# Performance work log

Measured on AMD Instinct MI355X. Metric: run time of the kernel, lower is better.

Reference implementation:

```python
import jax, jax.numpy as jnp
import numpy as np

PATCH_RATIO = 0.1
EPS = 1e-8

def _unfold(x, ps):
    # torch F.unfold(kernel=stride=ps): [b,c,H,W] -> [b, c*ps*ps, L], (c,kh,kw)-major channel layout
    b, c, H, W = x.shape
    nh, nw = (H - ps) // ps + 1, (W - ps) // ps + 1
    xc = x[:, :, :nh * ps, :nw * ps].reshape(b, c, nh, ps, nw, ps)
    u = xc.transpose(0, 1, 3, 5, 2, 4).reshape(b, c * ps * ps, nh * nw)
    return u, nh, nw

def _fold(cols, ps, H, W, nh, nw, c):
    # torch F.fold(kernel=stride=ps, output=(H,W)); non-overlapping so no accumulation,
    # uncovered bottom/right border is zero
    b = cols.shape[0]
    y = cols.reshape(b, c, ps, ps, nh, nw).transpose(0, 1, 4, 2, 5, 3)
    y = y.reshape(b, c, nh * ps, nw * ps)
    return jnp.pad(y, ((0, 0), (0, 0), (0, H - nh * ps), (0, W - nw * ps)))

def _forward(x, H, W):
    b, c = x.shape[0], x.shape[1]
    ps = min(int(H * PATCH_RATIO) + 1, int(W * PATCH_RATIO) + 1)
    u, nh, nw = _unfold(x, ps)                       # [b, c*ps*ps, L]
    p = nh * nw
    # faithful replication of the original (layout-scrambling) reshape
    x_p = u.reshape(b, ps * ps, c, p).transpose(0, 3, 2, 1)   # [b, p, c, ps*ps]
    g = jnp.mean(x, axis=(2, 3))                     # GAP -> [b, c]
    # cosine_similarity(x_g expanded, x_p) over flattened (c*ps*ps):
    # expanded gap row = g repeated ps*ps times -> dot = ps_sumfree einsum, ||g_exp|| = ||g||*ps
    dot = jnp.einsum('bpcd,bc->bp', x_p, g)          # [b, p]
    gnorm = jnp.linalg.norm(g, axis=1) * ps          # [b]
    pnorm = jnp.sqrt(jnp.sum(x_p * x_p, axis=(2, 3)))  # [b, p]
    cos = dot / jnp.maximum(gnorm[:, None] * pnorm, EPS)
    idx = jnp.argmax(cos, axis=1)                    # most similar patch (topk k=1)
    ids = jnp.argmin(cos, axis=1)                    # least similar patch (topk of -cos)
    bidx = jnp.arange(b)
    x_p = x_p.at[bidx, idx].set(x_p[bidx, ids])      # scatter swap
    cols = x_p.reshape(b, p, c * ps * ps).transpose(0, 2, 1)  # [b, c*ps*ps, p]
    mask = _fold(cols, ps, H, W, nh, nw, c)          # [b, c, H, W]
    return mask * x

def setup_inputs() -> dict:
    key = jax.random.key(0)
    x = jax.random.normal(key, (2, 256, 512, 512), dtype=jnp.float32)
    return {"x": x, "H": 512, "W": 512}

def reference(x, H, W):
    return _forward(x, H, W)
```

## Files before the change

kernel.cpp:

```cpp
#include <hip/hip_runtime.h>

#define BB 2
#define CC 256
#define HH 512
#define WW 512
#define PS 52
#define NW 9
#define NP 81
#define COV 468
#define PLANE (HH*WW)
#define CHW (CC*PLANE)
#define SP (PS*PS)

__global__ __launch_bounds__(256) void gap_kernel(const float* __restrict__ x,
                                                  float* __restrict__ gsum) {
    int plane = blockIdx.x;
    const float4* p = (const float4*)(x + (size_t)plane * PLANE);
    float acc = 0.f;
    for (int i = threadIdx.x; i < PLANE / 4; i += 256) {
        float4 v = p[i];
        acc += v.x + v.y + v.z + v.w;
    }
    __shared__ float red[256];
    red[threadIdx.x] = acc;
    __syncthreads();
    for (int s = 128; s > 0; s >>= 1) {
        if (threadIdx.x < s) red[threadIdx.x] += red[threadIdx.x + s];
        __syncthreads();
    }
    if (threadIdx.x == 0) gsum[plane] = red[0];
}

__global__ __launch_bounds__(256) void stats_kernel(const float* __restrict__ x,
                                                    float* __restrict__ T,
                                                    float* __restrict__ pn) {
    int cg = blockIdx.x;
    int l  = blockIdx.y;
    int b  = blockIdx.z;
    int ph = l / NW, pw = l - ph * NW;
    int tid = threadIdx.x;
    int wv = tid >> 6;

    __shared__ float Tpart[4][256];
    #pragma unroll
    for (int w = 0; w < 4; w++) Tpart[w][tid] = 0.f;
    __syncthreads();

    float pacc = 0.f;
    const float* base_b = x + (size_t)b * CHW + (size_t)(ph * PS) * WW + (pw * PS);
    for (int ci = 0; ci < 32; ci++) {
        int ch = cg * 32 + ci;
        const float* base = base_b + (size_t)ch * PLANE;
        float a = 0.f;
        for (unsigned s = tid; s < SP; s += 256) {
            unsigned kh = s / PS;
            unsigned kw = s - kh * PS;
            float v = base[kh * WW + kw];
            a += v;
            pacc += v * v;
        }
        int bin = (144 * ch + tid) & 255;
        Tpart[wv][bin] += a;
    }
    __syncthreads();

    float tsum = Tpart[0][tid] + Tpart[1][tid] + Tpart[2][tid] + Tpart[3][tid];
    T[(((size_t)b * NP + l) * 8 + cg) * 256 + tid] = tsum;

    __shared__ float red[256];
    red[tid] = pacc;
    __syncthreads();
    for (int s2 = 128; s2 > 0; s2 >>= 1) {
        if (tid < s2) red[tid] += red[tid + s2];
        __syncthreads();
    }
    if (tid == 0) pn[((size_t)b * NP + l) * 8 + cg] = red[0];
}

__global__ __launch_bounds__(256) void select_kernel(const float* __restrict__ gsum,
                                                     const float* __restrict__ T,
                                                     const float* __restrict__ pn,
                                                     int* __restrict__ sel) {
    int b = blockIdx.x;
    int t = threadIdx.x;
    float g = gsum[b * 256 + t] * (1.0f / PLANE);

    __shared__ float red[256];
    red[t] = g * g;
    __syncthreads();
    for (int s = 128; s > 0; s >>= 1) {
        if (t < s) red[t] += red[t + s];
        __syncthreads();
    }
    float gnorm = sqrtf(red[0]) * (float)PS;
    __syncthreads();

    float best = -1e30f, worst = 1e30f;
    int bi = 0, wi = 0;
    for (int l = 0; l < NP; l++) {
        const float* Tl = T + ((size_t)b * NP + l) * 8 * 256;
        float d = 0.f;
        #pragma unroll
        for (int cg = 0; cg < 8; cg++) d += Tl[cg * 256 + t];
        d *= g;
        red[t] = d;
        __syncthreads();
        for (int s = 128; s > 0; s >>= 1) {
            if (t < s) red[t] += red[t + s];
            __syncthreads();
        }
        if (t == 0) {
            float pacc = 0.f;
            #pragma unroll
            for (int cg = 0; cg < 8; cg++) pacc += pn[((size_t)b * NP + l) * 8 + cg];
            float pnorm = sqrtf(pacc);
            float cosv = red[0] / fmaxf(gnorm * pnorm, 1e-8f);
            if (cosv > best) { best = cosv; bi = l; }
            if (cosv < worst) { worst = cosv; wi = l; }
        }
        __syncthreads();
    }
    if (t == 0) { sel[b * 2 + 0] = bi; sel[b * 2 + 1] = wi; }
}

__global__ __launch_bounds__(256) void apply_kernel(const float* __restrict__ x,
                                                    float* __restrict__ out,
                                                    const int* __restrict__ sel) {
    int tile = blockIdx.x;
    int tc = tile / 43;
    int ts = tile - tc * 43;
    int l = blockIdx.y;
    int b = blockIdx.z;
    int ph = l / NW, pw = l - ph * NW;
    int idx = sel[b * 2 + 0], ids = sel[b * 2 + 1];
    int sl_patch = (l == idx) ? ids : l;
    int sph = sl_patch / NW, spw = sl_patch - sph * NW;

    const float* xb = x + (size_t)b * CHW;
    const float* src_base = xb + (size_t)(sph * PS) * WW + (spw * PS);

    __shared__ float tilebuf[64][65];
    int cb = tc * 64;
    int sb = ts * 64;
    int t = threadIdx.x;

    {
        int cl = t & 63;
        int sr = t >> 6;
        #pragma unroll
        for (int i = 0; i < 16; i++) {
            int s_l = i * 4 + sr;
            int s_g = sb + s_l;
            float v = 0.f;
            if (s_g < SP) {
                unsigned du = (unsigned)s_g * 256u + (unsigned)(cb + cl);
                unsigned chs = du / SP;
                unsigned rem = du - chs * SP;
                unsigned kh = rem / PS;
                unsigned kw = rem - kh * PS;
                v = src_base[(size_t)chs * PLANE + kh * WW + kw];
            }
            tilebuf[s_l][cl] = v;
        }
    }
    __syncthreads();
    {
        int sl = t & 63;
        int cr = t >> 6;
        int s_g = sb + sl;
        if (s_g < SP) {
            unsigned sh = (unsigned)s_g / PS;
            unsigned sw = (unsigned)s_g - sh * PS;
            size_t pos = (size_t)(ph * PS + sh) * WW + (pw * PS + sw);
            #pragma unroll
            for (int i = 0; i < 16; i++) {
                int c_l = i * 4 + cr;
                size_t off = (size_t)(cb + c_l) * PLANE + pos;
                out[(size_t)b * CHW + off] = tilebuf[sl][c_l] * xb[off];
            }
        }
    }
}

__global__ __launch_bounds__(256) void border_kernel(float* __restrict__ out) {
    int plane = blockIdx.y;
    int t = blockIdx.x * 256 + threadIdx.x;
    if (t >= 10780) return;
    float4* p = (float4*)(out + (size_t)plane * PLANE);
    int idx4;
    if (t < 5632) {
        int row = t / 11;
        int col = t - row * 11;
        idx4 = row * 128 + 117 + col;
    } else {
        int t2 = t - 5632;
        int row = t2 / 117;
        int col = t2 - row * 117;
        idx4 = (COV + row) * 128 + col;
    }
    p[idx4] = make_float4(0.f, 0.f, 0.f, 0.f);
}

extern "C" void kernel_launch(void* const* d_in, const int* in_sizes, int n_in,
                              void* d_out, int out_size, void* d_ws, size_t ws_size,
                              hipStream_t stream) {
    const float* x = (const float*)d_in[0];
    float* out = (float*)d_out;
    float* ws = (float*)d_ws;

    float* T    = ws;
    float* pn   = ws + 331776;
    float* gsum = ws + 333072;
    int*   sel  = (int*)(ws + 333584);

    gap_kernel<<<dim3(BB * CC), dim3(256), 0, stream>>>(x, gsum);
    stats_kernel<<<dim3(8, NP, BB), dim3(256), 0, stream>>>(x, T, pn);
    select_kernel<<<dim3(BB), dim3(256), 0, stream>>>(gsum, T, pn, sel);
    apply_kernel<<<dim3(172, NP, BB), dim3(256), 0, stream>>>(x, out, sel);
    border_kernel<<<dim3(43, BB * CC), dim3(256), 0, stream>>>(out);
}
```

Baseline: 1.424 ms.

## Fuse GAP, patch stats, masked output and border zeroing into single pass with fixup

```diff
diff --git a/kernel.cpp b/kernel.cpp
--- a/kernel.cpp
+++ b/kernel.cpp
@@ -12,134 +12,269 @@
 #define CHW (CC*PLANE)
 #define SP (PS*PS)
 
-__global__ __launch_bounds__(256) void gap_kernel(const float* __restrict__ x,
-                                                  float* __restrict__ gsum) {
-    int plane = blockIdx.x;
-    const float4* p = (const float4*)(x + (size_t)plane * PLANE);
-    float acc = 0.f;
-    for (int i = threadIdx.x; i < PLANE / 4; i += 256) {
-        float4 v = p[i];
-        acc += v.x + v.y + v.z + v.w;
-    }
-    __shared__ float red[256];
-    red[threadIdx.x] = acc;
+#define WS_S     0
+#define WS_PN    41472
+#define WS_GSUM  41634
+#define WS_ZTOT  42146
+#define WS_COS   42146
+#define WS_SEL   42308
+
+__global__ __launch_bounds__(256) void zero_kernel(float* __restrict__ ws) {
+    int i = blockIdx.x * 256 + threadIdx.x;
+    if (i < WS_ZTOT) ws[i] = 0.f;
+}
+
+__global__ __launch_bounds__(256) void mega_kernel(const float* __restrict__ x,
+                                                   float* __restrict__ out,
+                                                   float* __restrict__ S,
+                                                   float* __restrict__ pn,
+                                                   float* __restrict__ gsum) {
+    const int cg = blockIdx.x;
+    const int h  = blockIdx.y;
+    const int b  = blockIdx.z;
+    const int t  = threadIdx.x;
+    const int c2 = t >> 4;
+    const int wq = t & 15;
+    const int ch = cg * 16 + c2;
+    const float* xb = x + (size_t)b * CHW;
+    float* ob = out + (size_t)b * CHW;
+
+    const size_t rowoff = (size_t)ch * PLANE + (size_t)h * WW;
+    const float4* xrow = (const float4*)(xb + rowoff);
+    float4* orow = (float4*)(ob + rowoff);
+
+    float gacc = 0.f;
+
+    if (h >= COV) {
+        #pragma unroll
+        for (int i = 0; i < 8; i++) {
+            int w4 = wq + 16 * i;
+            float4 v = xrow[w4];
+            gacc += v.x + v.y + v.z + v.w;
+            orow[w4] = make_float4(0.f, 0.f, 0.f, 0.f);
+        }
+        #pragma unroll
+        for (int o = 8; o > 0; o >>= 1) gacc += __shfl_down(gacc, o, 16);
+        if (wq == 0) atomicAdd(gsum + b * CC + ch, gacc);
+        return;
+    }
+
+    const int ph = h / PS;
+    const int sh = h - ph * PS;
+    const int s0 = sh * PS;
+    const float* prow = xb + (size_t)(ph * PS) * WW;
+
+    float sacc[NW];
+    #pragma unroll
+    for (int p = 0; p < NW; p++) sacc[p] = 0.f;
+    float qacc = 0.f;
+
+    #pragma unroll
+    for (int i = 0; i < 8; i++) {
+        int w4 = wq + 16 * i;
+        float4 v = xrow[w4];
+        gacc += v.x + v.y + v.z + v.w;
+        float4 ov;
+        if (w4 < 117) {
+            float m[4];
+            #pragma unroll
+            for (int j = 0; j < 4; j++) {
+                int w = w4 * 4 + j;
+                int pw = w / PS;
+                int sw = w - pw * PS;
+                unsigned du  = (unsigned)(s0 + sw) * 256u + (unsigned)ch;
+                unsigned chs = du / (unsigned)SP;
+                unsigned rem = du - chs * (unsigned)SP;
+                unsigned kh  = rem / (unsigned)PS;
+                unsigned kw  = rem - kh * (unsigned)PS;
+                float g = prow[(size_t)chs * PLANE + pw * PS + kh * WW + kw];
+                m[j] = g;
+                sacc[pw] += g;
+                qacc += g * g;
+            }
+            ov.x = m[0] * v.x;
+            ov.y = m[1] * v.y;
+            ov.z = m[2] * v.z;
+            ov.w = m[3] * v.w;
+        } else {
+            ov = make_float4(0.f, 0.f, 0.f, 0.f);
+        }
+        orow[w4] = ov;
+    }
+
+    #pragma unroll
+    for (int o = 8; o > 0; o >>= 1) {
+        gacc += __shfl_down(gacc, o, 16);
+        qacc += __shfl_down(qacc, o, 16);
+        #pragma unroll
+        for (int p = 0; p < NW; p++) sacc[p] += __shfl_down(sacc[p], o, 16);
+    }
+    if (wq == 0) {
+        atomicAdd(gsum + b * CC + ch, gacc);
+        #pragma unroll
+        for (int p = 0; p < NW; p++)
+            atomicAdd(S + ((size_t)(b * NP + ph * NW + p)) * 256 + ch, sacc[p]);
+    } else if (wq == 1) {
+    }
+    if (wq == 0) {
+    }
+    (void)0;
+}
+
+
+__global__ __launch_bounds__(256) void mega_kernel2(const float* __restrict__ x,
+                                                    float* __restrict__ out,
+                                                    float* __restrict__ S,
+                                                    float* __restrict__ pn,
+                                                    float* __restrict__ gsum) {
+    const int cg = blockIdx.x;
+    const int h  = blockIdx.y;
+    const int b  = blockIdx.z;
+    const int t  = threadIdx.x;
+    const int c2 = t >> 4;
+    const int wq = t & 15;
+    const int ch = cg * 16 + c2;
+    const float* xb = x + (size_t)b * CHW;
+    float* ob = out + (size_t)b * CHW;
+
+    const size_t rowoff = (size_t)ch * PLANE + (size_t)h * WW;
+    const float4* xrow = (const float4*)(xb + rowoff);
+    float4* orow = (float4*)(ob + rowoff);
+
+    float gacc = 0.f;
+
+    if (h >= COV) {
+        #pragma unroll
+        for (int i = 0; i < 8; i++) {
+            int w4 = wq + 16 * i;
+            float4 v = xrow[w4];
+            gacc += v.x + v.y + v.z + v.w;
+            orow[w4] = make_float4(0.f, 0.f, 0.f, 0.f);
+        }
+        #pragma unroll
+        for (int o = 8; o > 0; o >>= 1) gacc += __shfl_down(gacc, o, 16);
+        if (wq == 0) atomicAdd(gsum + b * CC + ch, gacc);
+        return;
+    }
+
+    const int ph = h / PS;
+    const int sh = h - ph * PS;
+    const int s0 = sh * PS;
+    const float* prow = xb + (size_t)(ph * PS) * WW;
+
+    float sacc[NW], qpat[NW];
+    #pragma unroll
+    for (int p = 0; p < NW; p++) { sacc[p] = 0.f; qpat[p] = 0.f; }
+
+    #pragma unroll
+    for (int i = 0; i < 8; i++) {
+        int w4 = wq + 16 * i;
+        float4 v = xrow[w4];
+        gacc += v.x + v.y + v.z + v.w;
+        float4 ov;
+        if (w4 < 117) {
+            float m[4];
+            #pragma unroll
+            for (int j = 0; j < 4; j++) {
+                int w = w4 * 4 + j;
+                int pw = w / PS;
+                int sw = w - pw * PS;
+                unsigned du  = (unsigned)(s0 + sw) * 256u + (unsigned)ch;
+                unsigned chs = du / (unsigned)SP;
+                unsigned rem = du - chs * (unsigned)SP;
+                unsigned kh  = rem / (unsigned)PS;
+                unsigned kw  = rem - kh * (unsigned)PS;
+                float g = prow[(size_t)chs * PLANE + pw * PS + kh * WW + kw];
+                m[j] = g;
+                sacc[pw] += g;
+                qpat[pw] += g * g;
+            }
+            ov.x = m[0] * v.x;
+            ov.y = m[1] * v.y;
+            ov.z = m[2] * v.z;
+            ov.w = m[3] * v.w;
+        } else {
+            ov = make_float4(0.f, 0.f, 0.f, 0.f);
+        }
+        orow[w4] = ov;
+    }
+
+    #pragma unroll
+    for (int o = 8; o > 0; o >>= 1) {
+        gacc += __shfl_down(gacc, o, 16);
+        #pragma unroll
+        for (int p = 0; p < NW; p++) {
+            sacc[p] += __shfl_down(sacc[p], o, 16);
+            qpat[p] += __shfl_down(qpat[p], o, 16);
+        }
+    }
+    if (wq == 0) {
+        atomicAdd(gsum + b * CC + ch, gacc);
+        size_t Sbase = ((size_t)(b * NP + ph * NW)) * 256 + ch;
+        #pragma unroll
+        for (int p = 0; p < NW; p++) {
+            atomicAdd(S + Sbase + (size_t)p * 256, sacc[p]);
+            atomicAdd(pn + b * NP + ph * NW + p, qpat[p]);
+        }
+    }
+}
+
+__global__ __launch_bounds__(256) void cos_kernel(const float* __restrict__ gsum,
+                                                  const float* __restrict__ S,
+                                                  const float* __restrict__ pn,
+                                                  float* __restrict__ cosv) {
+    int l = blockIdx.x;
+    int b = blockIdx.y;
+    int t = threadIdx.x;
+    float g = gsum[b * CC + t] * (1.0f / PLANE);
+    float d  = S[((size_t)(b * NP + l)) * 256 + t] * g;
+    float gg = g * g;
+    #pragma unroll
+    for (int o = 32; o > 0; o >>= 1) { d += __shfl_down(d, o); gg += __shfl_down(gg, o); }
+    __shared__ float rd[4], rg[4];
+    int wv = t >> 6;
+    if ((t & 63) == 0) { rd[wv] = d; rg[wv] = gg; }
     __syncthreads();
-    for (int s = 128; s > 0; s >>= 1) {
-        if (threadIdx.x < s) red[threadIdx.x] += red[threadIdx.x + s];
-        __syncthreads();
-    }
-    if (threadIdx.x == 0) gsum[plane] = red[0];
-}
-
-__global__ __launch_bounds__(256) void stats_kernel(const float* __restrict__ x,
-                                                    float* __restrict__ T,
-                                                    float* __restrict__ pn) {
-    int cg = blockIdx.x;
-    int l  = blockIdx.y;
-    int b  = blockIdx.z;
-    int ph = l / NW, pw = l - ph * NW;
-    int tid = threadIdx.x;
-    int wv = tid >> 6;
-
-    __shared__ float Tpart[4][256];
-    #pragma unroll
-    for (int w = 0; w < 4; w++) Tpart[w][tid] = 0.f;
-    __syncthreads();
-
-    float pacc = 0.f;
-    const float* base_b = x + (size_t)b * CHW + (size_t)(ph * PS) * WW + (pw * PS);
-    for (int ci = 0; ci < 32; ci++) {
-        int ch = cg * 32 + ci;
-        const float* base = base_b + (size_t)ch * PLANE;
-        float a = 0.f;
-        for (unsigned s = tid; s < SP; s += 256) {
-            unsigned kh = s / PS;
-            unsigned kw = s - kh * PS;
-            float v = base[kh * WW + kw];
-            a += v;
-            pacc += v * v;
-        }
-        int bin = (144 * ch + tid) & 255;
-        Tpart[wv][bin] += a;
-    }
-    __syncthreads();
-
-    float tsum = Tpart[0][tid] + Tpart[1][tid] + Tpart[2][tid] + Tpart[3][tid];
-    T[(((size_t)b * NP + l) * 8 + cg) * 256 + tid] = tsum;
-
-    __shared__ float red[256];
-    red[tid] = pacc;
-    __syncthreads();
-    for (int s2 = 128; s2 > 0; s2 >>= 1) {
-        if (tid < s2) red[tid] += red[tid + s2];
-        __syncthreads();
-    }
-    if (tid == 0) pn[((size_t)b * NP + l) * 8 + cg] = red[0];
-}
-
-__global__ __launch_bounds__(256) void select_kernel(const float* __restrict__ gsum,
-                                                     const float* __restrict__ T,
-                                                     const float* __restrict__ pn,
-                                                     int* __restrict__ sel) {
-    int b = blockIdx.x;
-    int t = threadIdx.x;
-    float g = gsum[b * 256 + t] * (1.0f / PLANE);
-
-    __shared__ float red[256];
-    red[t] = g * g;
-    __syncthreads();
-    for (int s = 128; s > 0; s >>= 1) {
-        if (t < s) red[t] += red[t + s];
-        __syncthreads();
-    }
-    float gnorm = sqrtf(red[0]) * (float)PS;
-    __syncthreads();
-
-    float best = -1e30f, worst = 1e30f;
-    int bi = 0, wi = 0;
-    for (int l = 0; l < NP; l++) {
-        const float* Tl = T + ((size_t)b * NP + l) * 8 * 256;
-        float d = 0.f;
-        #pragma unroll
-        for (int cg = 0; cg < 8; cg++) d += Tl[cg * 256 + t];
-        d *= g;
-        red[t] = d;
-        __syncthreads();
-        for (int s = 128; s > 0; s >>= 1) {
-            if (t < s) red[t] += red[t + s];
-            __syncthreads();
-        }
-        if (t == 0) {
-            float pacc = 0.f;
-            #pragma unroll
-            for (int cg = 0; cg < 8; cg++) pacc += pn[((size_t)b * NP + l) * 8 + cg];
-            float pnorm = sqrtf(pacc);
-            float cosv = red[0] / fmaxf(gnorm * pnorm, 1e-8f);
-            if (cosv > best) { best = cosv; bi = l; }
-            if (cosv < worst) { worst = cosv; wi = l; }
-        }
-        __syncthreads();
-    }
-    if (t == 0) { sel[b * 2 + 0] = bi; sel[b * 2 + 1] = wi; }
-}
-
-__global__ __launch_bounds__(256) void apply_kernel(const float* __restrict__ x,
+    if (t == 0) {
+        float dt = rd[0] + rd[1] + rd[2] + rd[3];
+        float gt = rg[0] + rg[1] + rg[2] + rg[3];
+        float gnorm = sqrtf(gt) * (float)PS;
+        float pnorm = sqrtf(pn[b * NP + l]);
+        cosv[b * NP + l] = dt / fmaxf(gnorm * pnorm, 1e-8f);
+    }
+}
+
+__global__ void sel_kernel(const float* __restrict__ cosv, int* __restrict__ sel) {
+    int b = threadIdx.x;
+    if (b < BB) {
+        float best = -1e30f, worst = 1e30f;
+        int bi = 0, wi = 0;
+        for (int l = 0; l < NP; l++) {
+            float c = cosv[b * NP + l];
+            if (c > best)  { best  = c; bi = l; }
+            if (c < worst) { worst = c; wi = l; }
+        }
+        sel[b * 2 + 0] = bi;
+        sel[b * 2 + 1] = wi;
+    }
+}
+
+__global__ __launch_bounds__(256) void fixup_kernel(const float* __restrict__ x,
                                                     float* __restrict__ out,
                                                     const int* __restrict__ sel) {
-    int tile = blockIdx.x;
-    int tc = tile / 43;
-    int ts = tile - tc * 43;
-    int l = blockIdx.y;
-    int b = blockIdx.z;
+    int tile_i = blockIdx.x;
+    int tc = tile_i / 43;
+    int ts = tile_i - tc * 43;
+    int b = blockIdx.y;
+    int l = sel[b * 2 + 0];
+    int srcp = sel[b * 2 + 1];
     int ph = l / NW, pw = l - ph * NW;
-    int idx = sel[b * 2 + 0], ids = sel[b * 2 + 1];
-    int sl_patch = (l == idx) ? ids : l;
-    int sph = sl_patch / NW, spw = sl_patch - sph * NW;
+    int sph = srcp / NW, spw = srcp - sph * NW;
 
     const float* xb = x + (size_t)b * CHW;
     const float* src_base = xb + (size_t)(sph * PS) * WW + (spw * PS);
 
-    __shared__ float tilebuf[64][65];
+    __shared__ float tb[64][65];
     int cb = tc * 64;
     int sb = ts * 64;
     int t = threadIdx.x;
@@ -153,14 +288,14 @@
             int s_g = sb + s_l;
             float v = 0.f;
             if (s_g < SP) {
-                unsigned du = (unsigned)s_g * 256u + (unsigned)(cb + cl);
-                unsigned chs = du / SP;
-                unsigned rem = du - chs * SP;
-                unsigned kh = rem / PS;
-                unsigned kw = rem - kh * PS;
+                unsigned du  = (unsigned)s_g * 256u + (unsigned)(cb + cl);
+                unsigned chs = du / (unsigned)SP;
+                unsigned rem = du - chs * (unsigned)SP;
+                unsigned kh  = rem / (unsigned)PS;
+                unsigned kw  = rem - kh * (unsigned)PS;
                 v = src_base[(size_t)chs * PLANE + kh * WW + kw];
             }
-            tilebuf[s_l][cl] = v;
+            tb[s_l][cl] = v;
         }
     }
     __syncthreads();
@@ -169,36 +304,17 @@
         int cr = t >> 6;
         int s_g = sb + sl;
         if (s_g < SP) {
-            unsigned sh = (unsigned)s_g / PS;
-            unsigned sw = (unsigned)s_g - sh * PS;
-            size_t pos = (size_t)(ph * PS + sh) * WW + (pw * PS + sw);
+            unsigned shh = (unsigned)s_g / PS;
+            unsigned sww = (unsigned)s_g - shh * PS;
+            size_t pos = (size_t)(ph * PS + shh) * WW + (pw * PS + sww);
             #pragma unroll
             for (int i = 0; i < 16; i++) {
                 int c_l = i * 4 + cr;
                 size_t off = (size_t)(cb + c_l) * PLANE + pos;
-                out[(size_t)b * CHW + off] = tilebuf[sl][c_l] * xb[off];
+                out[(size_t)b * CHW + off] = tb[sl][c_l] * xb[off];
             }
         }
     }
-}
-
-__global__ __launch_bounds__(256) void border_kernel(float* __restrict__ out) {
-    int plane = blockIdx.y;
-    int t = blockIdx.x * 256 + threadIdx.x;
-    if (t >= 10780) return;
-    float4* p = (float4*)(out + (size_t)plane * PLANE);
-    int idx4;
-    if (t < 5632) {
-        int row = t / 11;
-        int col = t - row * 11;
-        idx4 = row * 128 + 117 + col;
-    } else {
-        int t2 = t - 5632;
-        int row = t2 / 117;
-        int col = t2 - row * 117;
-        idx4 = (COV + row) * 128 + col;
-    }
-    p[idx4] = make_float4(0.f, 0.f, 0.f, 0.f);
 }
 
 extern "C" void kernel_launch(void* const* d_in, const int* in_sizes, int n_in,
@@ -208,14 +324,15 @@
     float* out = (float*)d_out;
     float* ws = (float*)d_ws;
 
-    float* T    = ws;
-    float* pn   = ws + 331776;
-    float* gsum = ws + 333072;
-    int*   sel  = (int*)(ws + 333584);
-
-    gap_kernel<<<dim3(BB * CC), dim3(256), 0, stream>>>(x, gsum);
-    stats_kernel<<<dim3(8, NP, BB), dim3(256), 0, stream>>>(x, T, pn);
-    select_kernel<<<dim3(BB), dim3(256), 0, stream>>>(gsum, T, pn, sel);
-    apply_kernel<<<dim3(172, NP, BB), dim3(256), 0, stream>>>(x, out, sel);
-    border_kernel<<<dim3(43, BB * CC), dim3(256), 0, stream>>>(out);
-}
+    float* S    = ws + WS_S;
+    float* pn   = ws + WS_PN;
+    float* gsum = ws + WS_GSUM;
+    float* cosv = ws + WS_COS;
+    int*   sel  = (int*)(ws + WS_SEL);
+
+    zero_kernel<<<dim3((WS_ZTOT + 255) / 256), dim3(256), 0, stream>>>(ws);
+    mega_kernel2<<<dim3(16, HH, BB), dim3(256), 0, stream>>>(x, out, S, pn, gsum);
+    cos_kernel<<<dim3(NP, BB), dim3(256), 0, stream>>>(gsum, S, pn, cosv);
+    sel_kernel<<<dim3(1), dim3(64), 0, stream>>>(cosv, sel);
+    fixup_kernel<<<dim3(172, BB), dim3(256), 0, stream>>>(x, out, sel);
+}
```

Result: slower. 3.361 ms (+136.0%).
